# Performance work log

Hardware: AMD Instinct MI355X
Metric: run time of the kernel (lower is better)

The kernel has to match this reference:

```python
import jax, jax.numpy as jnp
import numpy as np

B, T = 256, 50
N_ITEMS = 100000
EMB = 256      # embedding
KBD = 128      # KBembedding == MN_dims
HID = 256      # layers[0] == layers[-1]
OUT = 256      # out_dim
NF = 10        # MN_nfactors == n_r


def setup_inputs() -> dict:
    key = jax.random.key(0)
    ks = jax.random.split(key, 18)
    s = 0.05
    return {
        "X": jax.random.randint(ks[0], (B, T), 0, N_ITEMS),
        "E": jax.random.normal(ks[1], (N_ITEMS, EMB), jnp.float32) * s,
        "KBE": jax.random.normal(ks[2], (N_ITEMS, KBD), jnp.float32) * s,
        "r_matrix": jax.random.normal(ks[3], (NF, KBD), jnp.float32) * s,
        "W_ih": jax.random.normal(ks[4], (3 * HID, EMB), jnp.float32) * s,
        "W_hh": jax.random.normal(ks[5], (3 * HID, HID), jnp.float32) * s,
        "b_ih": jnp.zeros((3 * HID,), jnp.float32),
        "b_hh": jnp.zeros((3 * HID,), jnp.float32),
        "MNu_W": jax.random.normal(ks[6], (KBD, HID), jnp.float32) * s,
        "MNu_b": jnp.zeros((KBD,), jnp.float32),
        "MNu2_W": jax.random.normal(ks[7], (HID, KBD + HID), jnp.float32) * s,
        "MNu2_b": jnp.zeros((HID,), jnp.float32),
        "MNea_W": jax.random.normal(ks[8], (KBD, KBD), jnp.float32) * s,
        "MNea_b": jnp.zeros((KBD,), jnp.float32),
        "mlp1_W": jax.random.normal(ks[9], (OUT, HID), jnp.float32) * s,
        "mlp1_b": jnp.zeros((OUT,), jnp.float32),
        "mlp2_W": jax.random.normal(ks[10], (OUT, EMB + KBD), jnp.float32) * s,
        "mlp2_b": jnp.zeros((OUT,), jnp.float32),
    }


def _gru_cell(x, h, W_ih, W_hh, b_ih, b_hh):
    # PyTorch GRUCell: gates stacked [r, z, n] along dim 0 of weights
    gi = x @ W_ih.T + b_ih
    gh = h @ W_hh.T + b_hh
    ir, iz, inn = jnp.split(gi, 3, axis=-1)
    hr, hz, hn = jnp.split(gh, 3, axis=-1)
    r = jax.nn.sigmoid(ir + hr)
    z = jax.nn.sigmoid(iz + hz)
    n = jnp.tanh(inn + r * hn)
    return (1.0 - z) * n + z * h


def reference(X, E, KBE, r_matrix, W_ih, W_hh, b_ih, b_hh,
              MNu_W, MNu_b, MNu2_W, MNu2_b, MNea_W, MNea_b,
              mlp1_W, mlp1_b, mlp2_W, mlp2_b):
    Bv, Tv = X.shape
    Em = E.at[0].set(0.0)     # mask row 0 of E
    KBm = KBE.at[0].set(0.0)  # mask row 0 of KBE
    Sx = Em[X]                # (B, T, EMB)
    KBItem = KBm[X]           # (B, T, KBD)

    def step(carry, xs):
        h, MN, y_sum = carry
        x_t, kb_t = xs                      # (B, EMB), (B, KBD)
        h = _gru_cell(x_t, h, W_ih, W_hh, b_ih, b_hh)
        y = h                                # dropout p=0 -> identity
        # gated memory write
        EA = jnp.tanh(kb_t @ MNea_W.T + MNea_b)          # (B, KBD)
        EA = EA[:, None, :] + r_matrix                    # (B, NF, KBD)
        gate = jax.nn.sigmoid(jnp.sum(MN * EA, axis=-1, keepdims=True))  # (B, NF, 1)
        MN = MN * (1.0 - gate) + EA * gate
        # attention read
        U = jnp.tanh(y @ MNu_W.T + MNu_b)                 # (B, KBD)
        AW = jax.nn.softmax(U @ r_matrix.T, axis=1)       # (B, NF)
        AC = jnp.einsum('bfd,bf->bd', MN, AW)             # (B, KBD)
        Ut = jnp.tanh(jnp.concatenate([y, AC], axis=-1) @ MNu2_W.T + MNu2_b)  # (B, HID)
        y_out = jnp.tanh(Ut @ mlp1_W.T + mlp1_b)          # (B, OUT)
        return (h, MN, y_sum + y_out), None

    init = (jnp.zeros((Bv, HID), Sx.dtype),
            jnp.zeros((Bv, NF, KBD), Sx.dtype),
            jnp.zeros((Bv, OUT), Sx.dtype))
    xs = (jnp.swapaxes(Sx, 0, 1), jnp.swapaxes(KBItem, 0, 1))  # (T, B, *)
    (h, MN, y_sum), _ = jax.lax.scan(step, init, xs)
    y = y_sum / Tv

    MergeE = jnp.concatenate([E, KBE], axis=1).at[0].set(0.0)  # (N, EMB+KBD)
    Sy = jnp.tanh(MergeE @ mlp2_W.T + mlp2_b)                  # (N, OUT)
    scores = jax.nn.log_softmax(y @ Sy.T, axis=1)              # (B, N)
    return scores, y
```

## Files before the change

### kernel.cpp

```cpp
#include <hip/hip_runtime.h>

typedef _Float16 f16;
typedef _Float16 f16x8 __attribute__((ext_vector_type(8)));
typedef float f32x4 __attribute__((ext_vector_type(4)));

#define MFMA16(a,b,c) __builtin_amdgcn_mfma_f32_16x16x32_f16(a,b,c,0,0,0)

#define NITEMS 100000
#define NBLK4  1563

#define OFF_WIH   0u
#define OFF_WHH   393216u
#define OFF_MNU   786432u
#define OFF_MNU2  851968u
#define OFF_MNEA  1048576u
#define OFF_MLP1  1081344u
#define OFF_MLP2  1212416u
#define OFF_GI    1409024u
#define OFF_TV    21069824u
#define OFF_MN    24346624u
#define OFF_YALL  57114624u
#define OFF_SY    66945024u
#define OFF_Y16   118407168u
#define OFF_PMAX  118538240u
#define OFF_PSUM  120176640u
#define OFF_LSE   121815040u

__device__ __forceinline__ float sigm(float x) { return 1.f / (1.f + __expf(-x)); }
__device__ __forceinline__ float tanh_fast(float x) {
  return 1.f - 2.f / (1.f + __expf(2.f * x));
}

__global__ __launch_bounds__(256) void k_pack(
    const float* s0, const float* s1, const float* s2, const float* s3,
    const float* s4, const float* s5, const float* s6, f16* base)
{
  int fid = blockIdx.x * 256 + threadIdx.x;
  const float* src; f16* dst; int K, f;
  if (fid < 24576)      { src = s0; dst = base;          K = 256; f = fid; }
  else if (fid < 49152) { src = s1; dst = base + 196608; K = 256; f = fid - 24576; }
  else if (fid < 53248) { src = s2; dst = base + 393216; K = 256; f = fid - 49152; }
  else if (fid < 65536) { src = s3; dst = base + 425984; K = 384; f = fid - 53248; }
  else if (fid < 67584) { src = s4; dst = base + 524288; K = 128; f = fid - 65536; }
  else if (fid < 75776) { src = s5; dst = base + 540672; K = 256; f = fid - 67584; }
  else                  { src = s6; dst = base + 606208; K = 384; f = fid - 75776; }
  int lane = f & 63, t2 = f >> 6, KS = K >> 5;
  int ks = t2 % KS, nt = t2 / KS;
  int row = nt * 16 + (lane & 15), col = ks * 32 + ((lane >> 4) << 3);
  const float* sp = src + (size_t)row * K + col;
  f16x8 v;
  #pragma unroll
  for (int j = 0; j < 8; j++) v[j] = (f16)sp[j];
  *(f16x8*)(dst + (size_t)f * 8) = v;
}

__global__ __launch_bounds__(512) void k_giea(
    const int* __restrict__ X, const float* __restrict__ E,
    const f16* __restrict__ Wih_p, const float* __restrict__ bih, f16* __restrict__ gi,
    const float* __restrict__ KBE, const f16* __restrict__ Wea_p,
    const float* __restrict__ bea, f16* __restrict__ tv)
{
  __shared__ __align__(16) f16 At[32][264];
  int tid = threadIdx.x;
  int w = tid >> 6, lane = tid & 63, lr = lane & 15, lg = lane >> 4;
  if (blockIdx.x < 400) {
    int r0 = blockIdx.x * 32;
    int t = r0 >> 8;
    {
      int r = tid >> 4, c = (tid & 15) * 16;
      int b = (r0 + r) & 255;
      int item = X[b * 50 + t];
      if (item == 0) {
        #pragma unroll
        for (int j = 0; j < 16; j++) At[r][c + j] = (f16)0.f;
      } else {
        const float4* sp = (const float4*)(E + (size_t)item * 256 + c);
        #pragma unroll
        for (int q = 0; q < 4; q++) {
          float4 v = sp[q];
          At[r][c + q*4 + 0] = (f16)v.x; At[r][c + q*4 + 1] = (f16)v.y;
          At[r][c + q*4 + 2] = (f16)v.z; At[r][c + q*4 + 3] = (f16)v.w;
        }
      }
    }
    __syncthreads();
    f32x4 acc[2][6] = {};
    for (int ks = 0; ks < 8; ks++) {
      f16x8 a0 = *(const f16x8*)(&At[lr][ks * 32 + lg * 8]);
      f16x8 a1 = *(const f16x8*)(&At[16 + lr][ks * 32 + lg * 8]);
      #pragma unroll
      for (int j = 0; j < 6; j++) {
        int nt = w * 6 + j;
        f16x8 bf = *(const f16x8*)(Wih_p + ((size_t)((nt * 8 + ks) * 64 + lane) << 3));
        acc[0][j] = MFMA16(a0, bf, acc[0][j]);
        acc[1][j] = MFMA16(a1, bf, acc[1][j]);
      }
    }
    #pragma unroll
    for (int j = 0; j < 6; j++) {
      int col = (w * 6 + j) * 16 + lr;
      float bias = bih[col];
      #pragma unroll
      for (int mt = 0; mt < 2; mt++)
        #pragma unroll
        for (int rr = 0; rr < 4; rr++) {
          int row = r0 + mt * 16 + lg * 4 + rr;
          gi[(size_t)row * 768 + col] = (f16)(acc[mt][j][rr] + bias);
        }
    }
  } else {
    int r0 = (blockIdx.x - 400) * 32;
    int t = r0 >> 8;
    {
      int r = tid >> 4, c = (tid & 15) * 8;
      int b = (r0 + r) & 255;
      int item = X[b * 50 + t];
      if (item == 0) {
        #pragma unroll
        for (int j = 0; j < 8; j++) At[r][c + j] = (f16)0.f;
      } else {
        const float4* sp = (const float4*)(KBE + (size_t)item * 128 + c);
        #pragma unroll
        for (int q = 0; q < 2; q++) {
          float4 v = sp[q];
          At[r][c + q*4 + 0] = (f16)v.x; At[r][c + q*4 + 1] = (f16)v.y;
          At[r][c + q*4 + 2] = (f16)v.z; At[r][c + q*4 + 3] = (f16)v.w;
        }
      }
    }
    __syncthreads();
    f32x4 acc[2] = {};
    for (int ks = 0; ks < 4; ks++) {
      f16x8 a0 = *(const f16x8*)(&At[lr][ks * 32 + lg * 8]);
      f16x8 a1 = *(const f16x8*)(&At[16 + lr][ks * 32 + lg * 8]);
      f16x8 bf = *(const f16x8*)(Wea_p + ((size_t)((w * 4 + ks) * 64 + lane) << 3));
      acc[0] = MFMA16(a0, bf, acc[0]);
      acc[1] = MFMA16(a1, bf, acc[1]);
    }
    int col = w * 16 + lr;
    float bias = bea[col];
    #pragma unroll
    for (int mt = 0; mt < 2; mt++)
      #pragma unroll
      for (int rr = 0; rr < 4; rr++) {
        int row = r0 + mt * 16 + lg * 4 + rr;
        tv[(size_t)row * 128 + col] = (f16)tanh_fast(acc[mt][rr] + bias);
      }
  }
}

__global__ __launch_bounds__(1024)
__attribute__((amdgpu_waves_per_eu(4, 4)))
void k_fused(
    const f16* __restrict__ Whh_p, const float* __restrict__ bhh,
    const f16* __restrict__ gi, f16* __restrict__ y_all,
    const f16* __restrict__ tv, const float* __restrict__ Rm, f16* __restrict__ MN,
    const float* __restrict__ E, const float* __restrict__ KBE,
    const f16* __restrict__ mlp2_p, const float* __restrict__ mlp2b, f16* __restrict__ Sy)
{
  __shared__ __align__(16) char smem[147456];
  int tid = threadIdx.x, w = tid >> 6, lane = tid & 63, lr = lane & 15, lg = lane >> 4;

  if (blockIdx.x < 32) {
    f16* Wlds = (f16*)smem;
    f16* hb0 = (f16*)(smem + 131072);
    f16* hb1 = (f16*)(smem + 139264);
    int r0 = blockIdx.x * 8;
    {
      const float4* src = (const float4*)Whh_p;
      float4* dst = (float4*)Wlds;
      #pragma unroll
      for (int i = 0; i < 8; i++) dst[tid + i * 1024] = src[tid + i * 1024];
      float4 z4 = {0.f, 0.f, 0.f, 0.f};
      ((float4*)hb0)[tid] = z4;
    }
    f16x8 Wz[8], Wn[8];
    #pragma unroll
    for (int ks = 0; ks < 8; ks++) {
      Wz[ks] = *(const f16x8*)(Whh_p + ((size_t)(((16 + w) * 8 + ks) * 64 + lane) << 3));
      Wn[ks] = *(const f16x8*)(Whh_p + ((size_t)(((32 + w) * 8 + ks) * 64 + lane) << 3));
      asm volatile("" : "+a"(Wz[ks]), "+a"(Wn[ks]));
    }
    int col = w * 16 + lr;
    float bR = bhh[col], bZ = bhh[col + 256], bN = bhh[col + 512];
    float hreg[4] = {0.f, 0.f, 0.f, 0.f};
    const f16* gP = gi + (size_t)(r0 + lg * 4) * 768 + col;
    f16 P[4][3];
    if (lg < 2) {
      #pragma unroll
      for (int rr = 0; rr < 4; rr++)
        #pragma unroll
        for (int g = 0; g < 3; g++)
          P[rr][g] = gP[rr * 768 + g * 256];
    }
    __syncthreads();
    f16* hc = hb0; f16* hn_ = hb1;
    int xr = (lr & 7) << 4;
    const f16* wB0 = Wlds + (size_t)w * 4096 + lane * 8;
    for (int t = 0; t < 50; t++) {
      f32x4 aR = {}, aZ = {}, aN = {};
      const char* hbase = (const char*)hc + lr * 512;
      #pragma unroll
      for (int ks = 0; ks < 8; ks++) {
        f16x8 a = *(const f16x8*)(hbase + ((ks * 64 + lg * 16) ^ xr));
        aR = MFMA16(a, *(const f16x8*)(wB0 + ks * 512), aR);
        aZ = MFMA16(a, Wz[ks], aZ);
        aN = MFMA16(a, Wn[ks], aN);
      }
      if (lg < 2) {
        #pragma unroll
        for (int rr = 0; rr < 4; rr++) {
          int row = lg * 4 + rr;
          float rg = sigm((float)P[rr][0] + aR[rr] + bR);
          float zg = sigm((float)P[rr][1] + aZ[rr] + bZ);
          float ng = tanh_fast((float)P[rr][2] + rg * (aN[rr] + bN));
          float hv = ng + zg * (hreg[rr] - ng);
          hreg[rr] = hv;
          *(f16*)((char*)hn_ + row * 512 + ((col * 2) ^ ((row & 7) << 4))) = (f16)hv;
        }
        if (t < 49) {
          const f16* gN = gP + (size_t)(t + 1) * 196608;
          #pragma unroll
          for (int rr = 0; rr < 4; rr++)
            #pragma unroll
            for (int g = 0; g < 3; g++)
              P[rr][g] = gN[rr * 768 + g * 256];
        }
      }
      __syncthreads();
      if (tid < 256) {
        int row = tid >> 5, c = tid & 31;
        f16x8 hv = *(const f16x8*)((char*)hn_ + row * 512 + ((c * 16) ^ ((row & 7) << 4)));
        *(f16x8*)(y_all + ((size_t)t * 256 + r0 + row) * 256 + c * 8) = hv;
      }
      f16* tmp = hc; hc = hn_; hn_ = tmp;
    }
  } else if (blockIdx.x < 192) {
    int pair = (blockIdx.x - 32) * 16 + w;
    int b = pair / 10, f = pair - (pair / 10) * 10;
    float r0_ = Rm[f * 128 + lane], r1_ = Rm[f * 128 + 64 + lane];
    float mn0 = 0.f, mn1 = 0.f;
    for (int t = 0; t < 50; t++) {
      size_t base = ((size_t)t * 256 + b) * 128;
      float ea0 = (float)tv[base + lane] + r0_;
      float ea1 = (float)tv[base + 64 + lane] + r1_;
      float p = mn0 * ea0 + mn1 * ea1;
      #pragma unroll
      for (int off = 32; off > 0; off >>= 1) p += __shfl_xor(p, off);
      float g = sigm(p);
      mn0 += (ea0 - mn0) * g;
      mn1 += (ea1 - mn1) * g;
      size_t mb = (((size_t)t * 256 + b) * 10 + f) * 128;
      MN[mb + lane] = (f16)mn0;
      MN[mb + 64 + lane] = (f16)mn1;
    }
  } else {
    f16* Ab0 = (f16*)smem;
    f16* Ab1 = (f16*)(smem + 25088);
    int bsy = blockIdx.x - 192;
    int r = tid >> 5, cE = (tid & 31) * 8, cK = (tid & 31) * 4;
    int mt = w & 1, ntp = w >> 1;
    float eE[8], eK[4];
    int tile = bsy;
    {
      int item = tile * 32 + r;
      if (item == 0) {
        #pragma unroll
        for (int j = 0; j < 8; j++) eE[j] = 0.f;
        #pragma unroll
        for (int j = 0; j < 4; j++) eK[j] = 0.f;
      } else {
        const float4* sp = (const float4*)(E + (size_t)item * 256 + cE);
        float4 v0 = sp[0], v1 = sp[1];
        eE[0]=v0.x; eE[1]=v0.y; eE[2]=v0.z; eE[3]=v0.w;
        eE[4]=v1.x; eE[5]=v1.y; eE[6]=v1.z; eE[7]=v1.w;
        float4 k0 = *(const float4*)(KBE + (size_t)item * 128 + cK);
        eK[0]=k0.x; eK[1]=k0.y; eK[2]=k0.z; eK[3]=k0.w;
      }
    }
    int cur = 0;
    while (tile < 3125) {
      f16* buf = cur ? Ab1 : Ab0;
      {
        f16* rowp = buf + r * 392;
        #pragma unroll
        for (int j = 0; j < 8; j++) rowp[cE + j] = (f16)eE[j];
        #pragma unroll
        for (int j = 0; j < 4; j++) rowp[256 + cK + j] = (f16)eK[j];
      }
      __syncthreads();
      int nxt = tile + 224;
      if (nxt < 3125) {
        int item = nxt * 32 + r;
        if (item == 0) {
          #pragma unroll
          for (int j = 0; j < 8; j++) eE[j] = 0.f;
          #pragma unroll
          for (int j = 0; j < 4; j++) eK[j] = 0.f;
        } else {
          const float4* sp = (const float4*)(E + (size_t)item * 256 + cE);
          float4 v0 = sp[0], v1 = sp[1];
          eE[0]=v0.x; eE[1]=v0.y; eE[2]=v0.z; eE[3]=v0.w;
          eE[4]=v1.x; eE[5]=v1.y; eE[6]=v1.z; eE[7]=v1.w;
          float4 k0 = *(const float4*)(KBE + (size_t)item * 128 + cK);
          eK[0]=k0.x; eK[1]=k0.y; eK[2]=k0.z; eK[3]=k0.w;
        }
      }
      int i0 = tile * 32;
      f32x4 acc[2] = {};
      for (int ks = 0; ks < 12; ks++) {
        f16x8 a = *(const f16x8*)(buf + (mt * 16 + lr) * 392 + ks * 32 + lg * 8);
        #pragma unroll
        for (int j = 0; j < 2; j++) {
          int nt = ntp * 2 + j;
          f16x8 bf = *(const f16x8*)(mlp2_p + ((size_t)((nt * 12 + ks) * 64 + lane) << 3));
          acc[j] = MFMA16(a, bf, acc[j]);
        }
      }
      #pragma unroll
      for (int j = 0; j < 2; j++) {
        int colS = (ntp * 2 + j) * 16 + lr;
        float bias = mlp2b[colS];
        #pragma unroll
        for (int rr = 0; rr < 4; rr++) {
          int item = i0 + mt * 16 + lg * 4 + rr;
          Sy[(size_t)item * 256 + colS] = (f16)tanh_fast(acc[j][rr] + bias);
        }
      }
      __syncthreads();
      tile = nxt; cur ^= 1;
    }
  }
}

__global__ __launch_bounds__(512) void k_uacut(
    const f16* __restrict__ y_all, const f16* __restrict__ MNu_p,
    const float* __restrict__ MNub, const float* __restrict__ Rm,
    const f16* __restrict__ MN,
    const f16* __restrict__ MNu2_p, const float* __restrict__ MNu2b,
    const f16* __restrict__ mlp1_p, const float* __restrict__ mlp1b,
    float* __restrict__ ypart)
{
  __shared__ __align__(16) char smem[25088];
  int tid = threadIdx.x, w = tid >> 6, lane = tid & 63, lr = lane & 15, lg = lane >> 4;
  f16   (*Aty)[264] = (f16(*)[264])smem;
  float (*Uf)[136]  = (float(*)[136])(smem + 8448);
  f16   (*Utl)[264] = (f16(*)[264])(smem + 8448);
  float (*Lg)[10]   = (float(*)[10])(smem + 17152);
  float (*Aw)[10]   = (float(*)[10])(smem + 17792);
  f16   (*ACs)[136] = (f16(*)[136])(smem + 18432);
  int r0 = blockIdx.x * 16;
  {
    int r = tid >> 5, c = (tid & 31) * 8;
    f16x8 v = *(const f16x8*)(y_all + (size_t)(r0 + r) * 256 + c);
    *(f16x8*)(&Aty[r][c]) = v;
  }
  __syncthreads();
  {
    f32x4 acc = {};
    for (int ks = 0; ks < 8; ks++) {
      f16x8 a = *(const f16x8*)(&Aty[lr][ks * 32 + lg * 8]);
      f16x8 bf = *(const f16x8*)(MNu_p + ((size_t)((w * 8 + ks) * 64 + lane) << 3));
      acc = MFMA16(a, bf, acc);
    }
    int col = w * 16 + lr;
    float bias = MNub[col];
    #pragma unroll
    for (int rr = 0; rr < 4; rr++)
      Uf[lg * 4 + rr][col] = tanh_fast(acc[rr] + bias);
  }
  __syncthreads();
  if (tid < 160) {
    int row = tid / 10, f = tid - (tid / 10) * 10;
    float s = 0.f;
    for (int d = 0; d < 128; d++) s += Uf[row][d] * Rm[f * 128 + d];
    Lg[row][f] = s;
  }
  __syncthreads();
  if (tid < 16) {
    float m = -1e30f;
    #pragma unroll
    for (int f = 0; f < 10; f++) m = fmaxf(m, Lg[tid][f]);
    float e[10], s = 0.f;
    #pragma unroll
    for (int f = 0; f < 10; f++) { e[f] = __expf(Lg[tid][f] - m); s += e[f]; }
    float inv = 1.f / s;
    #pragma unroll
    for (int f = 0; f < 10; f++) Aw[tid][f] = e[f] * inv;
  }
  __syncthreads();
  if (tid < 256) {
    int row = tid >> 4, d0 = (tid & 15) * 8;
    float a[8] = {0,0,0,0,0,0,0,0};
    for (int f = 0; f < 10; f++) {
      float wgt = Aw[row][f];
      f16x8 mv = *(const f16x8*)(MN + (((size_t)(r0 + row)) * 10 + f) * 128 + d0);
      #pragma unroll
      for (int q = 0; q < 8; q++) a[q] += wgt * (float)mv[q];
    }
    f16x8 o;
    #pragma unroll
    for (int q = 0; q < 8; q++) o[q] = (f16)a[q];
    *(f16x8*)(&ACs[row][d0]) = o;
  }
  __syncthreads();
  {
    f32x4 acc[2] = {};
    for (int ks = 0; ks < 12; ks++) {
      f16x8 a = (ks < 8)
        ? *(const f16x8*)(&Aty[lr][ks * 32 + lg * 8])
        : *(const f16x8*)(&ACs[lr][(ks - 8) * 32 + lg * 8]);
      #pragma unroll
      for (int j = 0; j < 2; j++) {
        f16x8 bf = *(const f16x8*)(MNu2_p + ((size_t)(((w * 2 + j) * 12 + ks) * 64 + lane) << 3));
        acc[j] = MFMA16(a, bf, acc[j]);
      }
    }
    __syncthreads();
    #pragma unroll
    for (int j = 0; j < 2; j++) {
      int col = (w * 2 + j) * 16 + lr;
      float bias = MNu2b[col];
      #pragma unroll
      for (int rr = 0; rr < 4; rr++)
        Utl[lg * 4 + rr][col] = (f16)tanh_fast(acc[j][rr] + bias);
    }
  }
  __syncthreads();
  {
    f32x4 acc2[2] = {};
    for (int ks = 0; ks < 8; ks++) {
      f16x8 a = *(const f16x8*)(&Utl[lr][ks * 32 + lg * 8]);
      #pragma unroll
      for (int j = 0; j < 2; j++) {
        f16x8 bf = *(const f16x8*)(mlp1_p + ((size_t)(((w * 2 + j) * 8 + ks) * 64 + lane) << 3));
        acc2[j] = MFMA16(a, bf, acc2[j]);
      }
    }
    #pragma unroll
    for (int j = 0; j < 2; j++) {
      int col = (w * 2 + j) * 16 + lr;
      float bias = mlp1b[col];
      #pragma unroll
      for (int rr = 0; rr < 4; rr++) {
        int row = r0 + lg * 4 + rr;
        ypart[(size_t)row * 256 + col] = tanh_fast(acc2[j][rr] + bias);
      }
    }
  }
}

__global__ __launch_bounds__(256) void k_yfin(
    const float* __restrict__ ypart, float* __restrict__ outy, f16* __restrict__ y16)
{
  int b = blockIdx.x, c = threadIdx.x;
  float s = 0.f;
  for (int t = 0; t < 50; t++) s += ypart[((size_t)t * 256 + b) * 256 + c];
  float v = s * (1.0f / 50.0f);
  outy[b * 256 + c] = v;
  y16[b * 256 + c] = (f16)v;
}

__global__ __launch_bounds__(512) void k_scoreraw(
    const f16* __restrict__ y16, const f16* __restrict__ Sy,
    float* __restrict__ pmax, float* __restrict__ psum, float* __restrict__ out)
{
  __shared__ __align__(16) char smx[70656];
  int tid = threadIdx.x, w = tid >> 6, lane = tid & 63, lr = lane & 15, lg = lane >> 4;
  int i0 = blockIdx.x * 64;
  int mtb = (w >> 1) * 4, ntb = (w & 1) * 2;
  f32x4 acc[4][2] = {};
  for (int ks = 0; ks < 8; ks++) {
    f16x8 a[4];
    #pragma unroll
    for (int i = 0; i < 4; i++)
      a[i] = *(const f16x8*)(y16 + ((size_t)((mtb + i) * 16 + lr)) * 256 + ks * 32 + lg * 8);
    #pragma unroll
    for (int j = 0; j < 2; j++) {
      int item = i0 + (ntb + j) * 16 + lr;
      int ic = item < NITEMS ? item : (NITEMS - 1);
      f16x8 bv = *(const f16x8*)(Sy + (size_t)ic * 256 + ks * 32 + lg * 8);
      #pragma unroll
      for (int i = 0; i < 4; i++) acc[i][j] = MFMA16(a[i], bv, acc[i][j]);
    }
  }
  float (*oS)[65] = (float(*)[65])smx;
  float* pm = (float*)(smx + 66560);
  float* ps = (float*)(smx + 68608);
  #pragma unroll
  for (int i = 0; i < 4; i++)
    #pragma unroll
    for (int j = 0; j < 2; j++)
      #pragma unroll
      for (int rr = 0; rr < 4; rr++) {
        int row = (mtb + i) * 16 + lg * 4 + rr;
        int c = (ntb + j) * 16 + lr;
        oS[row][c] = acc[i][j][rr];
      }
  {
    int item0 = i0 + ntb * 16 + lr, item1 = item0 + 16;
    bool v0 = item0 < NITEMS, v1 = item1 < NITEMS;
    #pragma unroll
    for (int i = 0; i < 4; i++)
      #pragma unroll
      for (int rr = 0; rr < 4; rr++) {
        float x0 = v0 ? acc[i][0][rr] : -1e30f;
        float x1 = v1 ? acc[i][1][rr] : -1e30f;
        float m = fmaxf(x0, x1);
        m = fmaxf(m, __shfl_xor(m, 1)); m = fmaxf(m, __shfl_xor(m, 2));
        m = fmaxf(m, __shfl_xor(m, 4)); m = fmaxf(m, __shfl_xor(m, 8));
        float s = (v0 ? __expf(x0 - m) : 0.f) + (v1 ? __expf(x1 - m) : 0.f);
        s += __shfl_xor(s, 1); s += __shfl_xor(s, 2);
        s += __shfl_xor(s, 4); s += __shfl_xor(s, 8);
        if (lr == 0) {
          int row = (mtb + i) * 16 + lg * 4 + rr;
          pm[(w & 1) * 256 + row] = m;
          ps[(w & 1) * 256 + row] = s;
        }
      }
  }
  __syncthreads();
  for (int it = 0; it < 32; it++) {
    int row = it * 8 + (tid >> 6);
    int c = tid & 63;
    if (i0 + c < NITEMS) out[(size_t)row * NITEMS + i0 + c] = oS[row][c];
  }
  if (tid < 256) {
    float m0 = pm[tid], m1 = pm[256 + tid];
    float s0 = ps[tid], s1 = ps[256 + tid];
    float M = fmaxf(m0, m1);
    float S = s0 * __expf(m0 - M) + s1 * __expf(m1 - M);
    pmax[(size_t)tid * 1600 + blockIdx.x] = M;
    psum[(size_t)tid * 1600 + blockIdx.x] = S;
  }
}

__global__ __launch_bounds__(256) void k_lse(
    const float* __restrict__ pmax, const float* __restrict__ psum, float* __restrict__ lse)
{
  int b = blockIdx.x, tid = threadIdx.x;
  __shared__ float red[256];
  float m = -1e30f;
  for (int i = tid; i < NBLK4; i += 256) m = fmaxf(m, pmax[(size_t)b * 1600 + i]);
  red[tid] = m; __syncthreads();
  for (int s = 128; s > 0; s >>= 1) {
    if (tid < s) red[tid] = fmaxf(red[tid], red[tid + s]);
    __syncthreads();
  }
  float M = red[0]; __syncthreads();
  float s = 0.f;
  for (int i = tid; i < NBLK4; i += 256)
    s += psum[(size_t)b * 1600 + i] * __expf(pmax[(size_t)b * 1600 + i] - M);
  red[tid] = s; __syncthreads();
  for (int q = 128; q > 0; q >>= 1) {
    if (tid < q) red[tid] += red[tid + q];
    __syncthreads();
  }
  if (tid == 0) lse[b] = M + logf(red[0]);
}

__global__ __launch_bounds__(256) void k_fix(
    float* __restrict__ out, const float* __restrict__ lse)
{
  int row = blockIdx.y;
  int idx = blockIdx.x * 256 + threadIdx.x;
  if (idx < 25000) {
    float l = lse[row];
    float4* p = (float4*)(out + (size_t)row * NITEMS) + idx;
    float4 v = *p;
    v.x -= l; v.y -= l; v.z -= l; v.w -= l;
    *p = v;
  }
}

extern "C" void kernel_launch(void* const* d_in, const int* in_sizes, int n_in,
                              void* d_out, int out_size, void* d_ws, size_t ws_size,
                              hipStream_t stream) {
  (void)in_sizes; (void)n_in; (void)out_size; (void)ws_size;
  const int*   X     = (const int*)d_in[0];
  const float* E     = (const float*)d_in[1];
  const float* KBE   = (const float*)d_in[2];
  const float* Rm    = (const float*)d_in[3];
  const float* Wih   = (const float*)d_in[4];
  const float* Whh   = (const float*)d_in[5];
  const float* bih   = (const float*)d_in[6];
  const float* bhh   = (const float*)d_in[7];
  const float* MNuW  = (const float*)d_in[8];
  const float* MNub  = (const float*)d_in[9];
  const float* MNu2W = (const float*)d_in[10];
  const float* MNu2b = (const float*)d_in[11];
  const float* MNeaW = (const float*)d_in[12];
  const float* MNeab = (const float*)d_in[13];
  const float* mlp1W = (const float*)d_in[14];
  const float* mlp1b = (const float*)d_in[15];
  const float* mlp2W = (const float*)d_in[16];
  const float* mlp2b = (const float*)d_in[17];

  char* ws = (char*)d_ws;
  f16*   Wih_p  = (f16*)(ws + OFF_WIH);
  f16*   Whh_p  = (f16*)(ws + OFF_WHH);
  f16*   MNu_p  = (f16*)(ws + OFF_MNU);
  f16*   MNu2_p = (f16*)(ws + OFF_MNU2);
  f16*   Wea_p  = (f16*)(ws + OFF_MNEA);
  f16*   mlp1_p = (f16*)(ws + OFF_MLP1);
  f16*   mlp2_p = (f16*)(ws + OFF_MLP2);
  f16*   gi     = (f16*)(ws + OFF_GI);
  f16*   tv     = (f16*)(ws + OFF_TV);
  f16*   MN     = (f16*)(ws + OFF_MN);
  f16*   y_all  = (f16*)(ws + OFF_YALL);
  f16*   Sy     = (f16*)(ws + OFF_SY);
  float* ypart  = (float*)(ws + OFF_GI);
  f16*   y16    = (f16*)(ws + OFF_Y16);
  float* pmax   = (float*)(ws + OFF_PMAX);
  float* psum   = (float*)(ws + OFF_PSUM);
  float* lse    = (float*)(ws + OFF_LSE);
  float* outf   = (float*)d_out;

  k_pack<<<344, 256, 0, stream>>>(Wih, Whh, MNuW, MNu2W, MNeaW, mlp1W, mlp2W, (f16*)ws);
  k_giea<<<800, 512, 0, stream>>>(X, E, Wih_p, bih, gi, KBE, Wea_p, MNeab, tv);
  k_fused<<<416, 1024, 0, stream>>>(Whh_p, bhh, gi, y_all, tv, Rm, MN,
                                    E, KBE, mlp2_p, mlp2b, Sy);
  k_uacut<<<800, 512, 0, stream>>>(y_all, MNu_p, MNub, Rm, MN,
                                   MNu2_p, MNu2b, mlp1_p, mlp1b, ypart);
  k_yfin<<<256, 256, 0, stream>>>(ypart, outf + 25600000, y16);
  k_scoreraw<<<NBLK4, 512, 0, stream>>>(y16, Sy, pmax, psum, outf);
  k_lse<<<256, 256, 0, stream>>>(pmax, psum, lse);
  dim3 gfix(98, 256);
  k_fix<<<gfix, 256, 0, stream>>>(outf, lse);
}
```

Baseline: 383.5 us.

## Restructure GRU recurrence to 16 rows per block with register-resident W_hh

```diff
diff --git a/kernel.cpp b/kernel.cpp
--- a/kernel.cpp
+++ b/kernel.cpp
@@ -56,19 +56,22 @@
 
 __global__ __launch_bounds__(512) void k_giea(
     const int* __restrict__ X, const float* __restrict__ E,
-    const f16* __restrict__ Wih_p, const float* __restrict__ bih, f16* __restrict__ gi,
+    const f16* __restrict__ Wih_p, const float* __restrict__ bih,
+    const float* __restrict__ bhh, f16* __restrict__ gi2,
     const float* __restrict__ KBE, const f16* __restrict__ Wea_p,
     const float* __restrict__ bea, f16* __restrict__ tv)
 {
-  __shared__ __align__(16) f16 At[32][264];
+  __shared__ __align__(16) char smem[66048];
   int tid = threadIdx.x;
   int w = tid >> 6, lane = tid & 63, lr = lane & 15, lg = lane >> 4;
+  f16 (*At)[264] = (f16(*)[264])smem;
   if (blockIdx.x < 400) {
-    int r0 = blockIdx.x * 32;
-    int t = r0 >> 8;
+    int r0g = blockIdx.x * 32;
+    int t = r0g >> 8;
+    int grp0 = (r0g & 255) >> 4;
     {
       int r = tid >> 4, c = (tid & 15) * 16;
-      int b = (r0 + r) & 255;
+      int b = (r0g + r) & 255;
       int item = X[b * 50 + t];
       if (item == 0) {
         #pragma unroll
@@ -96,17 +99,28 @@
         acc[1][j] = MFMA16(a1, bf, acc[1][j]);
       }
     }
+    f16* Lg2 = (f16*)(smem + 16896);
     #pragma unroll
     for (int j = 0; j < 6; j++) {
-      int col = (w * 6 + j) * 16 + lr;
-      float bias = bih[col];
+      int tile = w * 6 + j;
+      int gate = tile >> 4, rem = tile & 15;
+      int s2 = rem >> 2, ct2 = rem & 3;
+      int col = tile * 16 + lr;
+      float bias = bih[col] + (col < 512 ? bhh[col] : 0.f);
       #pragma unroll
       for (int mt = 0; mt < 2; mt++)
         #pragma unroll
-        for (int rr = 0; rr < 4; rr++) {
-          int row = r0 + mt * 16 + lg * 4 + rr;
-          gi[(size_t)row * 768 + col] = (f16)(acc[mt][j][rr] + bias);
-        }
+        for (int rr = 0; rr < 4; rr++)
+          Lg2[((mt * 4 + s2) * 64 + lane) * 48 + gate * 16 + ct2 * 4 + rr] =
+              (f16)(acc[mt][j][rr] + bias);
+    }
+    __syncthreads();
+    f16* dst = gi2 + (size_t)(t * 16 + grp0) * 12288;
+    #pragma unroll
+    for (int c = 0; c < 3; c++) {
+      int idx = (tid * 3 + c) * 8;
+      *(f16x8*)(dst + idx)         = *(const f16x8*)(Lg2 + idx);
+      *(f16x8*)(dst + 12288 + idx) = *(const f16x8*)(Lg2 + 12288 + idx);
     }
   } else {
     int r0 = (blockIdx.x - 400) * 32;
@@ -149,101 +163,223 @@
   }
 }
 
-__global__ __launch_bounds__(1024)
-__attribute__((amdgpu_waves_per_eu(4, 4)))
+__global__ __launch_bounds__(256)
+__attribute__((amdgpu_waves_per_eu(1, 1)))
 void k_fused(
     const f16* __restrict__ Whh_p, const float* __restrict__ bhh,
-    const f16* __restrict__ gi, f16* __restrict__ y_all,
+    const f16* __restrict__ gi2, f16* __restrict__ y_all,
     const f16* __restrict__ tv, const float* __restrict__ Rm, f16* __restrict__ MN,
     const float* __restrict__ E, const float* __restrict__ KBE,
     const f16* __restrict__ mlp2_p, const float* __restrict__ mlp2b, f16* __restrict__ Sy)
 {
-  __shared__ __align__(16) char smem[147456];
+  __shared__ __align__(16) char smem[50176];
   int tid = threadIdx.x, w = tid >> 6, lane = tid & 63, lr = lane & 15, lg = lane >> 4;
 
-  if (blockIdx.x < 32) {
-    f16* Wlds = (f16*)smem;
-    f16* hb0 = (f16*)(smem + 131072);
-    f16* hb1 = (f16*)(smem + 139264);
-    int r0 = blockIdx.x * 8;
+  if (blockIdx.x < 16) {
+    f16* hb0 = (f16*)smem;
+    f16* hb1 = (f16*)(smem + 8192);
+    int grp = blockIdx.x, r0 = grp * 16;
     {
-      const float4* src = (const float4*)Whh_p;
-      float4* dst = (float4*)Wlds;
-      #pragma unroll
-      for (int i = 0; i < 8; i++) dst[tid + i * 1024] = src[tid + i * 1024];
       float4 z4 = {0.f, 0.f, 0.f, 0.f};
-      ((float4*)hb0)[tid] = z4;
-    }
-    f16x8 Wz[8], Wn[8];
-    #pragma unroll
-    for (int ks = 0; ks < 8; ks++) {
-      Wz[ks] = *(const f16x8*)(Whh_p + ((size_t)(((16 + w) * 8 + ks) * 64 + lane) << 3));
-      Wn[ks] = *(const f16x8*)(Whh_p + ((size_t)(((32 + w) * 8 + ks) * 64 + lane) << 3));
-      asm volatile("" : "+a"(Wz[ks]), "+a"(Wn[ks]));
-    }
-    int col = w * 16 + lr;
-    float bR = bhh[col], bZ = bhh[col + 256], bN = bhh[col + 512];
-    float hreg[4] = {0.f, 0.f, 0.f, 0.f};
-    const f16* gP = gi + (size_t)(r0 + lg * 4) * 768 + col;
-    f16 P[4][3];
-    if (lg < 2) {
-      #pragma unroll
-      for (int rr = 0; rr < 4; rr++)
-        #pragma unroll
-        for (int g = 0; g < 3; g++)
-          P[rr][g] = gP[rr * 768 + g * 256];
-    }
+      float4* p = (float4*)smem;
+      p[tid] = z4; p[tid + 256] = z4; p[tid + 512] = z4; p[tid + 768] = z4;
+    }
+    f16x8 Wf[3][4][8];
+    #pragma unroll
+    for (int g = 0; g < 3; g++)
+      #pragma unroll
+      for (int ct = 0; ct < 4; ct++)
+        #pragma unroll
+        for (int ks = 0; ks < 8; ks++) {
+          int nt = g * 16 + w * 4 + ct;
+          Wf[g][ct][ks] = *(const f16x8*)(Whh_p + ((size_t)((nt * 8 + ks) * 64 + lane) << 3));
+        }
+    #pragma unroll
+    for (int g = 0; g < 3; g++)
+      #pragma unroll
+      for (int ct = 0; ct < 4; ct++)
+        #pragma unroll
+        for (int ks = 0; ks < 8; ks++)
+          asm volatile("" : "+v"(Wf[g][ct][ks]));
+    float bN[4];
+    #pragma unroll
+    for (int ct = 0; ct < 4; ct++) bN[ct] = bhh[512 + w * 64 + ct * 16 + lr];
+    float hreg[4][4] = {};
+    const f16* gP = gi2 + ((size_t)(grp * 4 + w) * 64 + lane) * 48;
     __syncthreads();
     f16* hc = hb0; f16* hn_ = hb1;
     int xr = (lr & 7) << 4;
-    const f16* wB0 = Wlds + (size_t)w * 4096 + lane * 8;
     for (int t = 0; t < 50; t++) {
-      f32x4 aR = {}, aZ = {}, aN = {};
+      const f16* gT = gP + (size_t)t * 196608;
       const char* hbase = (const char*)hc + lr * 512;
+      f16x8 Pa = *(const f16x8*)(gT);
+      f16x8 Pb = *(const f16x8*)(gT + 8);
+      f32x4 acc[4] = {};
       #pragma unroll
       for (int ks = 0; ks < 8; ks++) {
         f16x8 a = *(const f16x8*)(hbase + ((ks * 64 + lg * 16) ^ xr));
-        aR = MFMA16(a, *(const f16x8*)(wB0 + ks * 512), aR);
-        aZ = MFMA16(a, Wz[ks], aZ);
-        aN = MFMA16(a, Wn[ks], aN);
-      }
-      if (lg < 2) {
+        #pragma unroll
+        for (int ct = 0; ct < 4; ct++) acc[ct] = MFMA16(a, Wf[0][ct][ks], acc[ct]);
+      }
+      float rg[4][4];
+      f16x8 Pza = *(const f16x8*)(gT + 16);
+      f16x8 Pzb = *(const f16x8*)(gT + 24);
+      #pragma unroll
+      for (int ct = 0; ct < 4; ct++)
         #pragma unroll
         for (int rr = 0; rr < 4; rr++) {
-          int row = lg * 4 + rr;
-          float rg = sigm((float)P[rr][0] + aR[rr] + bR);
-          float zg = sigm((float)P[rr][1] + aZ[rr] + bZ);
-          float ng = tanh_fast((float)P[rr][2] + rg * (aN[rr] + bN));
-          float hv = ng + zg * (hreg[rr] - ng);
-          hreg[rr] = hv;
+          float p = (float)((ct < 2) ? Pa[ct * 4 + rr] : Pb[(ct - 2) * 4 + rr]);
+          rg[ct][rr] = sigm(p + acc[ct][rr]);
+        }
+      #pragma unroll
+      for (int ct = 0; ct < 4; ct++) acc[ct] = (f32x4){0.f, 0.f, 0.f, 0.f};
+      #pragma unroll
+      for (int ks = 0; ks < 8; ks++) {
+        f16x8 a = *(const f16x8*)(hbase + ((ks * 64 + lg * 16) ^ xr));
+        #pragma unroll
+        for (int ct = 0; ct < 4; ct++) acc[ct] = MFMA16(a, Wf[1][ct][ks], acc[ct]);
+      }
+      float zg[4][4];
+      f16x8 Pna = *(const f16x8*)(gT + 32);
+      f16x8 Pnb = *(const f16x8*)(gT + 40);
+      #pragma unroll
+      for (int ct = 0; ct < 4; ct++)
+        #pragma unroll
+        for (int rr = 0; rr < 4; rr++) {
+          float p = (float)((ct < 2) ? Pza[ct * 4 + rr] : Pzb[(ct - 2) * 4 + rr]);
+          zg[ct][rr] = sigm(p + acc[ct][rr]);
+        }
+      #pragma unroll
+      for (int ct = 0; ct < 4; ct++) acc[ct] = (f32x4){0.f, 0.f, 0.f, 0.f};
+      #pragma unroll
+      for (int ks = 0; ks < 8; ks++) {
+        f16x8 a = *(const f16x8*)(hbase + ((ks * 64 + lg * 16) ^ xr));
+        #pragma unroll
+        for (int ct = 0; ct < 4; ct++) acc[ct] = MFMA16(a, Wf[2][ct][ks], acc[ct]);
+      }
+      #pragma unroll
+      for (int ct = 0; ct < 4; ct++)
+        #pragma unroll
+        for (int rr = 0; rr < 4; rr++) {
+          float p = (float)((ct < 2) ? Pna[ct * 4 + rr] : Pnb[(ct - 2) * 4 + rr]);
+          float ng = tanh_fast(p + rg[ct][rr] * (acc[ct][rr] + bN[ct]));
+          float hv = ng + zg[ct][rr] * (hreg[ct][rr] - ng);
+          hreg[ct][rr] = hv;
+          int row = lg * 4 + rr, col = w * 64 + ct * 16 + lr;
           *(f16*)((char*)hn_ + row * 512 + ((col * 2) ^ ((row & 7) << 4))) = (f16)hv;
         }
-        if (t < 49) {
-          const f16* gN = gP + (size_t)(t + 1) * 196608;
+      __syncthreads();
+      {
+        int row = tid >> 4, c = (tid & 15) * 2;
+        f16x8 v0 = *(const f16x8*)((char*)hn_ + row * 512 + ((c * 16) ^ ((row & 7) << 4)));
+        f16x8 v1 = *(const f16x8*)((char*)hn_ + row * 512 + (((c + 1) * 16) ^ ((row & 7) << 4)));
+        f16* dst = y_all + ((size_t)t * 256 + r0 + row) * 256 + c * 8;
+        *(f16x8*)dst = v0; *(f16x8*)(dst + 8) = v1;
+      }
+      f16* tmp = hc; hc = hn_; hn_ = tmp;
+    }
+  } else if (blockIdx.x < 96) {
+    f16* Ab0 = (f16*)smem;
+    f16* Ab1 = (f16*)(smem + 25088);
+    int r = tid >> 3, sub = tid & 7;
+    int cE = sub * 32, cK = sub * 16;
+    int mt = w & 1, ntb = (w >> 1) * 8;
+    float eE[32], eK[16];
+    int tile = blockIdx.x - 16;
+    {
+      int item = tile * 32 + r;
+      if (item == 0) {
+        #pragma unroll
+        for (int j = 0; j < 32; j++) eE[j] = 0.f;
+        #pragma unroll
+        for (int j = 0; j < 16; j++) eK[j] = 0.f;
+      } else {
+        const float4* sp = (const float4*)(E + (size_t)item * 256 + cE);
+        #pragma unroll
+        for (int q = 0; q < 8; q++) {
+          float4 v = sp[q];
+          eE[q*4+0]=v.x; eE[q*4+1]=v.y; eE[q*4+2]=v.z; eE[q*4+3]=v.w;
+        }
+        const float4* kp = (const float4*)(KBE + (size_t)item * 128 + cK);
+        #pragma unroll
+        for (int q = 0; q < 4; q++) {
+          float4 v = kp[q];
+          eK[q*4+0]=v.x; eK[q*4+1]=v.y; eK[q*4+2]=v.z; eK[q*4+3]=v.w;
+        }
+      }
+    }
+    int cur = 0;
+    while (tile < 3125) {
+      f16* buf = cur ? Ab1 : Ab0;
+      {
+        f16* rowp = buf + r * 392;
+        #pragma unroll
+        for (int j = 0; j < 32; j++) rowp[cE + j] = (f16)eE[j];
+        #pragma unroll
+        for (int j = 0; j < 16; j++) rowp[256 + cK + j] = (f16)eK[j];
+      }
+      __syncthreads();
+      int nxt = tile + 80;
+      if (nxt < 3125) {
+        int item = nxt * 32 + r;
+        if (item == 0) {
           #pragma unroll
-          for (int rr = 0; rr < 4; rr++)
-            #pragma unroll
-            for (int g = 0; g < 3; g++)
-              P[rr][g] = gN[rr * 768 + g * 256];
+          for (int j = 0; j < 32; j++) eE[j] = 0.f;
+          #pragma unroll
+          for (int j = 0; j < 16; j++) eK[j] = 0.f;
+        } else {
+          const float4* sp = (const float4*)(E + (size_t)item * 256 + cE);
+          #pragma unroll
+          for (int q = 0; q < 8; q++) {
+            float4 v = sp[q];
+            eE[q*4+0]=v.x; eE[q*4+1]=v.y; eE[q*4+2]=v.z; eE[q*4+3]=v.w;
+          }
+          const float4* kp = (const float4*)(KBE + (size_t)item * 128 + cK);
+          #pragma unroll
+          for (int q = 0; q < 4; q++) {
+            float4 v = kp[q];
+            eK[q*4+0]=v.x; eK[q*4+1]=v.y; eK[q*4+2]=v.z; eK[q*4+3]=v.w;
+          }
+        }
+      }
+      int i0 = tile * 32;
+      f32x4 acc[8] = {};
+      for (int ks = 0; ks < 12; ks++) {
+        f16x8 a = *(const f16x8*)(buf + (mt * 16 + lr) * 392 + ks * 32 + lg * 8);
+        #pragma unroll
+        for (int j = 0; j < 8; j++) {
+          f16x8 bf = *(const f16x8*)(mlp2_p + ((size_t)(((ntb + j) * 12 + ks) * 64 + lane) << 3));
+          acc[j] = MFMA16(a, bf, acc[j]);
+        }
+      }
+      #pragma unroll
+      for (int j = 0; j < 8; j++) {
+        int colS = (ntb + j) * 16 + lr;
+        float bias = mlp2b[colS];
+        #pragma unroll
+        for (int rr = 0; rr < 4; rr++) {
+          int item = i0 + mt * 16 + lg * 4 + rr;
+          Sy[(size_t)item * 256 + colS] = (f16)tanh_fast(acc[j][rr] + bias);
         }
       }
       __syncthreads();
-      if (tid < 256) {
-        int row = tid >> 5, c = tid & 31;
-        f16x8 hv = *(const f16x8*)((char*)hn_ + row * 512 + ((c * 16) ^ ((row & 7) << 4)));
-        *(f16x8*)(y_all + ((size_t)t * 256 + r0 + row) * 256 + c * 8) = hv;
-      }
-      f16* tmp = hc; hc = hn_; hn_ = tmp;
-    }
-  } else if (blockIdx.x < 192) {
-    int pair = (blockIdx.x - 32) * 16 + w;
+      tile = nxt; cur ^= 1;
+    }
+  } else {
+    int pair = (blockIdx.x - 96) * 4 + w;
     int b = pair / 10, f = pair - (pair / 10) * 10;
     float r0_ = Rm[f * 128 + lane], r1_ = Rm[f * 128 + 64 + lane];
     float mn0 = 0.f, mn1 = 0.f;
+    float c0 = (float)tv[(size_t)b * 128 + lane];
+    float c1 = (float)tv[(size_t)b * 128 + 64 + lane];
     for (int t = 0; t < 50; t++) {
-      size_t base = ((size_t)t * 256 + b) * 128;
-      float ea0 = (float)tv[base + lane] + r0_;
-      float ea1 = (float)tv[base + 64 + lane] + r1_;
+      float ea0 = c0 + r0_;
+      float ea1 = c1 + r1_;
+      if (t < 49) {
+        size_t nb = ((size_t)(t + 1) * 256 + b) * 128;
+        c0 = (float)tv[nb + lane];
+        c1 = (float)tv[nb + 64 + lane];
+      }
       float p = mn0 * ea0 + mn1 * ea1;
       #pragma unroll
       for (int off = 32; off > 0; off >>= 1) p += __shfl_xor(p, off);
@@ -253,82 +389,6 @@
       size_t mb = (((size_t)t * 256 + b) * 10 + f) * 128;
       MN[mb + lane] = (f16)mn0;
       MN[mb + 64 + lane] = (f16)mn1;
-    }
-  } else {
-    f16* Ab0 = (f16*)smem;
-    f16* Ab1 = (f16*)(smem + 25088);
-    int bsy = blockIdx.x - 192;
-    int r = tid >> 5, cE = (tid & 31) * 8, cK = (tid & 31) * 4;
-    int mt = w & 1, ntp = w >> 1;
-    float eE[8], eK[4];
-    int tile = bsy;
-    {
-      int item = tile * 32 + r;
-      if (item == 0) {
-        #pragma unroll
-        for (int j = 0; j < 8; j++) eE[j] = 0.f;
-        #pragma unroll
-        for (int j = 0; j < 4; j++) eK[j] = 0.f;
-      } else {
-        const float4* sp = (const float4*)(E + (size_t)item * 256 + cE);
-        float4 v0 = sp[0], v1 = sp[1];
-        eE[0]=v0.x; eE[1]=v0.y; eE[2]=v0.z; eE[3]=v0.w;
-        eE[4]=v1.x; eE[5]=v1.y; eE[6]=v1.z; eE[7]=v1.w;
-        float4 k0 = *(const float4*)(KBE + (size_t)item * 128 + cK);
-        eK[0]=k0.x; eK[1]=k0.y; eK[2]=k0.z; eK[3]=k0.w;
-      }
-    }
-    int cur = 0;
-    while (tile < 3125) {
-      f16* buf = cur ? Ab1 : Ab0;
-      {
-        f16* rowp = buf + r * 392;
-        #pragma unroll
-        for (int j = 0; j < 8; j++) rowp[cE + j] = (f16)eE[j];
-        #pragma unroll
-        for (int j = 0; j < 4; j++) rowp[256 + cK + j] = (f16)eK[j];
-      }
-      __syncthreads();
-      int nxt = tile + 224;
-      if (nxt < 3125) {
-        int item = nxt * 32 + r;
-        if (item == 0) {
-          #pragma unroll
-          for (int j = 0; j < 8; j++) eE[j] = 0.f;
-          #pragma unroll
-          for (int j = 0; j < 4; j++) eK[j] = 0.f;
-        } else {
-          const float4* sp = (const float4*)(E + (size_t)item * 256 + cE);
-          float4 v0 = sp[0], v1 = sp[1];
-          eE[0]=v0.x; eE[1]=v0.y; eE[2]=v0.z; eE[3]=v0.w;
-          eE[4]=v1.x; eE[5]=v1.y; eE[6]=v1.z; eE[7]=v1.w;
-          float4 k0 = *(const float4*)(KBE + (size_t)item * 128 + cK);
-          eK[0]=k0.x; eK[1]=k0.y; eK[2]=k0.z; eK[3]=k0.w;
-        }
-      }
-      int i0 = tile * 32;
-      f32x4 acc[2] = {};
-      for (int ks = 0; ks < 12; ks++) {
-        f16x8 a = *(const f16x8*)(buf + (mt * 16 + lr) * 392 + ks * 32 + lg * 8);
-        #pragma unroll
-        for (int j = 0; j < 2; j++) {
-          int nt = ntp * 2 + j;
-          f16x8 bf = *(const f16x8*)(mlp2_p + ((size_t)((nt * 12 + ks) * 64 + lane) << 3));
-          acc[j] = MFMA16(a, bf, acc[j]);
-        }
-      }
-      #pragma unroll
-      for (int j = 0; j < 2; j++) {
-        int colS = (ntp * 2 + j) * 16 + lr;
-        float bias = mlp2b[colS];
-        #pragma unroll
-        for (int rr = 0; rr < 4; rr++) {
-          int item = i0 + mt * 16 + lg * 4 + rr;
-          Sy[(size_t)item * 256 + colS] = (f16)tanh_fast(acc[j][rr] + bias);
-        }
-      }
-      __syncthreads();
-      tile = nxt; cur ^= 1;
     }
   }
 }
@@ -604,7 +664,7 @@
   f16*   Wea_p  = (f16*)(ws + OFF_MNEA);
   f16*   mlp1_p = (f16*)(ws + OFF_MLP1);
   f16*   mlp2_p = (f16*)(ws + OFF_MLP2);
-  f16*   gi     = (f16*)(ws + OFF_GI);
+  f16*   gi2    = (f16*)(ws + OFF_GI);
   f16*   tv     = (f16*)(ws + OFF_TV);
   f16*   MN     = (f16*)(ws + OFF_MN);
   f16*   y_all  = (f16*)(ws + OFF_YALL);
@@ -617,9 +677,9 @@
   float* outf   = (float*)d_out;
 
   k_pack<<<344, 256, 0, stream>>>(Wih, Whh, MNuW, MNu2W, MNeaW, mlp1W, mlp2W, (f16*)ws);
-  k_giea<<<800, 512, 0, stream>>>(X, E, Wih_p, bih, gi, KBE, Wea_p, MNeab, tv);
-  k_fused<<<416, 1024, 0, stream>>>(Whh_p, bhh, gi, y_all, tv, Rm, MN,
-                                    E, KBE, mlp2_p, mlp2b, Sy);
+  k_giea<<<800, 512, 0, stream>>>(X, E, Wih_p, bih, bhh, gi2, KBE, Wea_p, MNeab, tv);
+  k_fused<<<736, 256, 0, stream>>>(Whh_p, bhh, gi2, y_all, tv, Rm, MN,
+                                   E, KBE, mlp2_p, mlp2b, Sy);
   k_uacut<<<800, 512, 0, stream>>>(y_all, MNu_p, MNub, Rm, MN,
                                    MNu2_p, MNu2b, mlp1_p, mlp1b, ypart);
   k_yfin<<<256, 256, 0, stream>>>(ypart, outf + 25600000, y16);
```

New measurement: 635.4 us. 65.7% more time.
